# Kernel tuning notes

Measured on AMD Instinct MI355X. Metric: run time of the kernel, lower is better.

## Reference

```python
import jax, jax.numpy as jnp
import numpy as np
import math

B = 65536
N_NUM = 64; N_CAT = 16; CAT_SIZE = 1000; EMB = 16
ND = 64; NA = 64; OUT = ND + NA; NSTEPS = 5; GAMMA = 1.5
NFEAT = N_NUM + N_CAT * EMB          # 320
NGROUPS = N_NUM + N_CAT              # 80
GROUP_IDX = np.repeat(np.arange(NGROUPS), [1] * N_NUM + [EMB] * N_CAT)  # len 320
RES_SCALE = math.sqrt(0.5)
BN_EPS = 1e-5


def setup_inputs() -> dict:
    keys = iter(jax.random.split(jax.random.key(0), 64))
    def rn(shape, std):
        return jax.random.normal(next(keys), shape, jnp.float32) * std
    def mk_bn(c, lead=()):
        # stacked (scale, bias, running_mean, running_var) along axis -2
        s = 1.0 + 0.05 * jax.random.normal(next(keys), (*lead, c), jnp.float32)
        b = 0.05 * jax.random.normal(next(keys), (*lead, c), jnp.float32)
        m = 0.05 * jax.random.normal(next(keys), (*lead, c), jnp.float32)
        v = 1.0 + 0.1 * jax.random.uniform(next(keys), (*lead, c), dtype=jnp.float32)
        return jnp.stack([s, b, m, v], axis=-2)
    inp = {}
    inp["x_num"] = jax.random.normal(next(keys), (B, N_NUM), jnp.float32)
    inp["x_cat"] = jax.random.randint(next(keys), (B, N_CAT), 0, CAT_SIZE)
    inp["emb_W"] = rn((N_CAT, CAT_SIZE, EMB), 0.1)
    inp["in_bn"] = mk_bn(NFEAT)
    inp["sh_W0"] = rn((NFEAT, 2 * OUT), 1.0 / math.sqrt(NFEAT))
    inp["sh_b0"] = jnp.zeros((2 * OUT,), jnp.float32)
    inp["sh_bn0"] = mk_bn(2 * OUT)
    inp["sh_W1"] = rn((OUT, 2 * OUT), 1.0 / math.sqrt(OUT))
    inp["sh_b1"] = jnp.zeros((2 * OUT,), jnp.float32)
    inp["sh_bn1"] = mk_bn(2 * OUT)
    inp["init_W"] = rn((2, OUT, 2 * OUT), 1.0 / math.sqrt(OUT))
    inp["init_b"] = jnp.zeros((2, 2 * OUT), jnp.float32)
    inp["init_bn"] = mk_bn(2 * OUT, (2,))
    inp["step_W"] = rn((NSTEPS, 2, OUT, 2 * OUT), 1.0 / math.sqrt(OUT))
    inp["step_b"] = jnp.zeros((NSTEPS, 2, 2 * OUT), jnp.float32)
    inp["step_bn"] = mk_bn(2 * OUT, (NSTEPS, 2))
    inp["att_W"] = rn((NSTEPS, NA, NGROUPS), 1.0 / math.sqrt(NA))
    inp["att_b"] = jnp.zeros((NSTEPS, NGROUPS), jnp.float32)
    inp["att_bn"] = mk_bn(NGROUPS, (NSTEPS,))
    inp["out_W"] = rn((ND, 1), 1.0 / math.sqrt(ND))
    inp["out_b"] = jnp.zeros((1,), jnp.float32)
    return inp


def bn_apply(x, p):
    s, b, m, v = p  # each [C]
    return (x - m) * jax.lax.rsqrt(v + BN_EPS) * s + b


def glu_layer(x, W, b, bn):
    h = bn_apply(x @ W + b, bn)          # [B, 2*OUT]
    o, g = jnp.split(h, 2, axis=1)
    return o * jax.nn.sigmoid(g)


def glu_block(x, W, b, bn):
    y = glu_layer(x, W, b, bn)
    return (x + y) * RES_SCALE if x.shape == y.shape else y


def sparsemax(z):
    # along axis=1; Martins & Astudillo 2016
    zs = -jnp.sort(-z, axis=1)
    cs = jnp.cumsum(zs, axis=1)
    r = jnp.arange(1, z.shape[1] + 1, dtype=z.dtype)
    support = (1.0 + r * zs) > cs
    k = jnp.maximum(support.sum(axis=1, keepdims=True), 1)
    cs_k = jnp.take_along_axis(cs, k - 1, axis=1)
    tau = (cs_k - 1.0) / k.astype(z.dtype)
    return jnp.maximum(z - tau, 0.0)


def _forward(x_num, x_cat, emb_W, in_bn, sh_W0, sh_b0, sh_bn0, sh_W1, sh_b1, sh_bn1,
             init_W, init_b, init_bn, step_W, step_b, step_bn, att_W, att_b, att_bn,
             out_W, out_b):
    # categorical embeddings: [B, N_CAT, EMB] -> [B, N_CAT*EMB]
    emb = emb_W[np.arange(N_CAT)[None, :], x_cat].reshape(x_cat.shape[0], -1)
    x = jnp.concatenate([x_num, emb], axis=1)  # [B, NFEAT]
    x = bn_apply(x, in_bn)

    def ft_shared(h):
        h = glu_block(h, sh_W0, sh_b0, sh_bn0)   # 320 -> 128, no residual
        return glu_block(h, sh_W1, sh_b1, sh_bn1)  # residual

    def ft_indep(h, W, b, bn):
        for i in range(W.shape[0]):
            h = glu_block(h, W[i], b[i], bn[i])
        return h

    out0 = ft_indep(ft_shared(x), init_W, init_b, init_bn)
    a = out0[:, ND:]
    prior = jnp.ones((x.shape[0], NGROUPS), x.dtype)
    decision_sum = jnp.zeros((x.shape[0], ND), x.dtype)
    for step in range(NSTEPS):
        logits = bn_apply(a @ att_W[step] + att_b[step], att_bn[step]) * prior
        mask_group = sparsemax(logits)           # [B, NGROUPS]
        prior = prior * (GAMMA - mask_group)
        mask = mask_group[:, GROUP_IDX]          # [B, NFEAT] (repeat_interleave)
        out = ft_indep(ft_shared(mask * x), step_W[step], step_b[step], step_bn[step])
        d, a = out[:, :ND], out[:, ND:]
        decision_sum = decision_sum + jax.nn.relu(d)
    return decision_sum @ out_W + out_b          # [B, 1]


def reference(x_num, x_cat, emb_W, in_bn, sh_W0, sh_b0, sh_bn0, sh_W1, sh_b1, sh_bn1,
              init_W, init_b, init_bn, step_W, step_b, step_bn, att_W, att_b, att_bn,
              out_W, out_b):
    return _forward(x_num, x_cat, emb_W, in_bn, sh_W0, sh_b0, sh_bn0, sh_W1, sh_b1,
                    sh_bn1, init_W, init_b, init_bn, step_W, step_b, step_bn,
                    att_W, att_b, att_bn, out_W, out_b)
```

## Files before the change

### kernel.cpp

```cpp
#include <hip/hip_runtime.h>
#include <math.h>
#include <stdint.h>

typedef _Float16 half_t;
typedef _Float16 half8 __attribute__((ext_vector_type(8)));
typedef float floatx4 __attribute__((ext_vector_type(4)));
typedef float floatx16 __attribute__((ext_vector_type(16)));

constexpr float BN_EPS_C = 1e-5f;
constexpr float RES_SCALE_C = 0.70710678118654752f;
constexpr float GAMMA_C = 1.5f;
#define B_TOT 65536

__device__ __forceinline__ uint32_t pack2(float y) {
    const half_t h = (half_t)y;
    const half_t l = (half_t)(y - (float)h);
    union { half_t f; unsigned short u; } a, b; a.f = h; b.f = l;
    return (uint32_t)a.u | ((uint32_t)b.u << 16);
}
__device__ __forceinline__ void unpack2(uint32_t v, half_t& h, half_t& l) {
    union { unsigned short u; half_t f; } a, b;
    a.u = (unsigned short)(v & 0xffffu); b.u = (unsigned short)(v >> 16);
    h = a.f; l = b.f;
}

__global__ void wsplit_kernel(const float* __restrict__ sh_W0, const float* __restrict__ sh_W1,
                              const float* __restrict__ init_W, const float* __restrict__ step_W,
                              half_t* __restrict__ Wh, half_t* __restrict__ Wl)
{
    const int b = blockIdx.x, n = threadIdx.x;
    const float* src; int k; size_t base;
    if (b < 320)      { src = sh_W0;           k = b;       base = 0; }
    else if (b < 448) { src = sh_W1;           k = b - 320; base = 81920; }
    else if (b < 576) { src = init_W;          k = b - 448; base = 114688; }
    else if (b < 704) { src = init_W + 32768;  k = b - 576; base = 147456; }
    else {
        int j = (b - 704) >> 7; k = (b - 704) & 127;
        src = step_W + (size_t)j * 32768; base = 180224 + (size_t)j * 32768;
    }
    const float v = src[k * 256 + n];
    const half_t hi = (half_t)v;
    const half_t lo = (half_t)(v - (float)hi);
    const size_t idx = base + (size_t)(((k >> 3) * 256 + n) * 8 + (k & 7));
    Wh[idx] = hi; Wl[idx] = lo;
}

__global__ void wsplit_att_kernel(const float* __restrict__ att_W,
                                  half_t* __restrict__ aWh, half_t* __restrict__ aWl)
{
    const int b = blockIdx.x;
    const int n = threadIdx.x;
    const int step = b >> 6, k = b & 63;
    const float v = att_W[(size_t)b * 80 + n];
    const half_t h = (half_t)v;
    const half_t l = (half_t)(v - (float)h);
    const size_t idx = (size_t)step * 5120 + (size_t)(((k >> 3) * 80 + n) * 8 + (k & 7));
    aWh[idx] = h; aWl[idx] = l;
}

__global__ void embed_bn_kernel(const float* __restrict__ x_num, const int* __restrict__ x_cat,
                                const float* __restrict__ emb_W, const float* __restrict__ in_bn,
                                uint32_t* __restrict__ xp)
{
    const int idx = blockIdx.x * 256 + threadIdx.x;
    const int s = idx / 320, j = idx - s * 320;
    float v;
    if (j < 64) v = x_num[(size_t)s * 64 + j];
    else {
        const int c = (j - 64) >> 4, e = (j - 64) & 15;
        v = emb_W[(size_t)(c * 1000 + x_cat[(size_t)s * 16 + c]) * 16 + e];
    }
    const float val = (v - in_bn[640 + j]) * (in_bn[j] * __frsqrt_rn(in_bn[960 + j] + BN_EPS_C)) + in_bn[320 + j];
    xp[idx] = pack2(val);
}

__device__ __forceinline__ void bn_fold(const float* __restrict__ bn, const float* __restrict__ bias,
                                        int c, float& sc, float& sh)
{
    sc = bn[c] * __frsqrt_rn(bn[768 + c] + BN_EPS_C);
    sh = fmaf(bias[c] - bn[512 + c], sc, bn[256 + c]);
}

__device__ __forceinline__ float glu_val(float accO, float accG,
                                         float sc_o, float sh_o, float sc_g, float sh_g)
{
    const float o = fmaf(accO, sc_o, sh_o);
    const float g = fmaf(accG, sc_g, sh_g);
    const float e = __expf(-g);
    return o * __builtin_amdgcn_rcpf(1.f + e);
}

#define MFMA32(A, B, C) C = __builtin_amdgcn_mfma_f32_32x32x16_f16(A, B, C, 0, 0, 0)
#define MFMA16(A, B, C) C = __builtin_amdgcn_mfma_f32_16x16x32_f16(A, B, C, 0, 0, 0)

__device__ __forceinline__ void layer_accum(const half_t (*H_h)[136], const half_t (*H_l)[136],
                                            const half_t* __restrict__ Wh, const half_t* __restrict__ Wl,
                                            size_t off, int n32, int k8, int no, int rot,
                                            floatx16* accO, floatx16* accG)
{
#pragma unroll 1
    for (int s = 0; s < 8; ++s) {
        const int sl8 = (s + rot) & 7;
        const int kq = sl8 * 2 + k8;
        const size_t wo = off + (size_t)(kq * 256 + no + n32) * 8;
        const half8 bo_h = *(const half8*)(Wh + wo);
        const half8 bo_l = *(const half8*)(Wl + wo);
        const half8 bg_h = *(const half8*)(Wh + wo + 1024);
        const half8 bg_l = *(const half8*)(Wl + wo + 1024);
#pragma unroll
        for (int mt = 0; mt < 4; ++mt) {
            const half8 a_h = *(const half8*)&H_h[mt * 32 + n32][sl8 * 16 + k8 * 8];
            const half8 a_l = *(const half8*)&H_l[mt * 32 + n32][sl8 * 16 + k8 * 8];
            MFMA32(a_h, bo_h, accO[mt]); MFMA32(a_h, bg_h, accG[mt]);
            MFMA32(a_l, bo_h, accO[mt]); MFMA32(a_l, bg_h, accG[mt]);
            MFMA32(a_h, bo_l, accO[mt]); MFMA32(a_h, bg_l, accG[mt]);
        }
    }
}

template<bool MASK>
__global__ __launch_bounds__(256, 2)
void ft_chain(const uint32_t* __restrict__ xp, uint32_t* __restrict__ avp,
              const half_t* __restrict__ Wh, const half_t* __restrict__ Wl,
              const half_t* __restrict__ aWh, const half_t* __restrict__ aWl,
              const float* __restrict__ att_b, const float* __restrict__ att_bn,
              float* __restrict__ prior,
              const float* __restrict__ b1, const float* __restrict__ bn1,
              const float* __restrict__ b2, const float* __restrict__ bn2,
              const float* __restrict__ b3, const float* __restrict__ bn3,
              const float* __restrict__ b4, const float* __restrict__ bn4,
              size_t w3_off, size_t w4_off,
              float* __restrict__ ds, int wmode_last, int step)
{
    __shared__ __align__(16) char smem[79872];
    float    (*mgs)[84]  = (float    (*)[84])smem;
    half_t   (*As_h)[72] = (half_t   (*)[72])(smem + 43008);
    half_t   (*As_l)[72] = (half_t   (*)[72])(smem + 61440);
    uint32_t (*Apk)[68]  = (uint32_t (*)[68])(smem + 43008);
    half_t   (*H_h)[136] = (half_t   (*)[136])smem;
    half_t   (*H_l)[136] = (half_t   (*)[136])(smem + 34816);

    const int t = threadIdx.x;
    const int s0 = blockIdx.x * 128;
    const int w = t >> 6, lane = t & 63;
    const int n32 = lane & 31, k8 = lane >> 5;
    const int quad = lane >> 4, l16 = lane & 15;
    const int no = 32 * w;
    const int half_id = (blockIdx.x >> 8) & 1;
    const int row = t >> 1, k0 = (t & 1) * 32;

    if (MASK) {
        {
            const uint4* src = (const uint4*)(avp + (size_t)(s0 + row) * 64 + k0);
            uint4* dst = (uint4*)&Apk[row][k0];
#pragma unroll
            for (int q = 0; q < 8; ++q) dst[q] = src[q];
        }
        __syncthreads();
        floatx4 zacc[2][5];
#pragma unroll
        for (int mt = 0; mt < 2; ++mt)
#pragma unroll
            for (int nt = 0; nt < 5; ++nt) zacc[mt][nt] = (floatx4){0.f, 0.f, 0.f, 0.f};
#pragma unroll
        for (int kc = 0; kc < 64; kc += 32) {
            half8 a_h[2], a_l[2];
#pragma unroll
            for (int mt = 0; mt < 2; ++mt) {
                uint32_t wv[8];
                *(uint4*)&wv[0] = *(const uint4*)&Apk[w * 32 + mt * 16 + l16][kc + quad * 8];
                *(uint4*)&wv[4] = *(const uint4*)&Apk[w * 32 + mt * 16 + l16][kc + quad * 8 + 4];
#pragma unroll
                for (int j = 0; j < 8; ++j) { half_t h, l; unpack2(wv[j], h, l); a_h[mt][j] = h; a_l[mt][j] = l; }
            }
            const int kq = (kc >> 3) + quad;
#pragma unroll
            for (int nt = 0; nt < 5; ++nt) {
                const size_t wi = (size_t)(kq * 80 + nt * 16 + l16) * 8;
                const half8 b_h = *(const half8*)(aWh + wi);
                const half8 b_l = *(const half8*)(aWl + wi);
#pragma unroll
                for (int mt = 0; mt < 2; ++mt) {
                    MFMA16(a_h[mt], b_h, zacc[mt][nt]);
                    MFMA16(a_l[mt], b_h, zacc[mt][nt]);
                    MFMA16(a_h[mt], b_l, zacc[mt][nt]);
                }
            }
        }
        float preg[2][5][4];
#pragma unroll
        for (int nt = 0; nt < 5; ++nt) {
            const int c = nt * 16 + l16;
            const float sc = att_bn[c] * __frsqrt_rn(att_bn[240 + c] + BN_EPS_C);
            const float sh = fmaf(att_b[c] - att_bn[160 + c], sc, att_bn[80 + c]);
#pragma unroll
            for (int mt = 0; mt < 2; ++mt)
#pragma unroll
                for (int r = 0; r < 4; ++r) {
                    const int sl = w * 32 + mt * 16 + quad * 4 + r;
                    const float pr = (step == 0) ? 1.f : prior[(size_t)(s0 + sl) * 80 + c];
                    preg[mt][nt][r] = pr;
                    mgs[sl][c] = fmaf(zacc[mt][nt][r], sc, sh) * pr;
                }
        }
        __syncthreads();
        {
            const int samp = row, j0 = (t & 1) * 40;
            float zj[40], zmax = -1e30f;
#pragma unroll
            for (int j = 0; j < 40; ++j) { zj[j] = mgs[samp][j0 + j]; zmax = fmaxf(zmax, zj[j]); }
            zmax = fmaxf(zmax, __shfl_xor(zmax, 1));
            float lo = zmax - 1.f, hi = zmax;
#pragma unroll 1
            for (int it = 0; it < 22; ++it) {
                const float mid = 0.5f * (lo + hi);
                float ssum = 0.f;
#pragma unroll
                for (int j = 0; j < 40; ++j) ssum += fmaxf(zj[j] - mid, 0.f);
                ssum += __shfl_xor(ssum, 1);
                if (ssum >= 1.f) lo = mid; else hi = mid;
            }
            const float tau = 0.5f * (lo + hi);
#pragma unroll
            for (int j = 0; j < 40; ++j) mgs[samp][j0 + j] = fmaxf(zj[j] - tau, 0.f);
        }
        __syncthreads();
#pragma unroll
        for (int nt = 0; nt < 5; ++nt) {
            const int c = nt * 16 + l16;
#pragma unroll
            for (int mt = 0; mt < 2; ++mt)
#pragma unroll
                for (int r = 0; r < 4; ++r) {
                    const int sl = w * 32 + mt * 16 + quad * 4 + r;
                    prior[(size_t)(s0 + sl) * 80 + c] = preg[mt][nt][r] * (GAMMA_C - mgs[sl][c]);
                }
        }
    }

    floatx16 accO[4], accG[4];
#pragma unroll
    for (int i = 0; i < 4; ++i) { accO[i] = (floatx16)(0.f); accG[i] = (floatx16)(0.f); }

    const uint32_t* arow = xp + (size_t)(s0 + row) * 320 + k0;
    uint32_t pfw[32];
    int ic = half_id * 2;
#pragma unroll
    for (int q = 0; q < 8; ++q)
        *(uint4*)&pfw[q * 4] = *(const uint4*)(arow + ic * 64 + q * 4);

#pragma unroll 1
    for (int i = 0; i < 5; ++i) {
        __syncthreads();
        {
            const int kb = ic * 64 + k0;
            float mA = 1.f, mB = 1.f;
            if (MASK && ic != 0) {
                mA = mgs[row][64 + ((kb - 64) >> 4)];
                mB = mgs[row][64 + ((kb - 48) >> 4)];
            }
#pragma unroll
            for (int q = 0; q < 4; ++q) {
                half8 hh, ll;
                if (MASK && ic == 0) {
                    const float4 m0q = *(const float4*)&mgs[row][kb + q * 8];
                    const float4 m1q = *(const float4*)&mgs[row][kb + q * 8 + 4];
                    const float mm[8] = {m0q.x, m0q.y, m0q.z, m0q.w, m1q.x, m1q.y, m1q.z, m1q.w};
#pragma unroll
                    for (int j = 0; j < 8; ++j) {
                        half_t h, l; unpack2(pfw[q * 8 + j], h, l);
                        const float v = ((float)h + (float)l) * mm[j];
                        const half_t nh = (half_t)v;
                        hh[j] = nh; ll[j] = (half_t)(v - (float)nh);
                    }
                } else if (MASK) {
                    const float m = (q < 2) ? mA : mB;
#pragma unroll
                    for (int j = 0; j < 8; ++j) {
                        half_t h, l; unpack2(pfw[q * 8 + j], h, l);
                        const float v = ((float)h + (float)l) * m;
                        const half_t nh = (half_t)v;
                        hh[j] = nh; ll[j] = (half_t)(v - (float)nh);
                    }
                } else {
#pragma unroll
                    for (int j = 0; j < 8; ++j) { half_t h, l; unpack2(pfw[q * 8 + j], h, l); hh[j] = h; ll[j] = l; }
                }
                *(half8*)&As_h[row][k0 + q * 8] = hh;
                *(half8*)&As_l[row][k0 + q * 8] = ll;
            }
        }
        __syncthreads();
        const int icn = (ic + 1 == 5) ? 0 : ic + 1;
        if (i < 4) {
#pragma unroll
            for (int q = 0; q < 8; ++q)
                *(uint4*)&pfw[q * 4] = *(const uint4*)(arow + icn * 64 + q * 4);
        }
#pragma unroll
        for (int sl4 = 0; sl4 < 4; ++sl4) {
            const int kq = ic * 8 + sl4 * 2 + k8;
            const size_t wo = (size_t)(kq * 256 + no + n32) * 8;
            const half8 bo_h = *(const half8*)(Wh + wo);
            const half8 bo_l = *(const half8*)(Wl + wo);
            const half8 bg_h = *(const half8*)(Wh + wo + 1024);
            const half8 bg_l = *(const half8*)(Wl + wo + 1024);
#pragma unroll
            for (int mt = 0; mt < 4; ++mt) {
                const half8 a_h = *(const half8*)&As_h[mt * 32 + n32][sl4 * 16 + k8 * 8];
                const half8 a_l = *(const half8*)&As_l[mt * 32 + n32][sl4 * 16 + k8 * 8];
                MFMA32(a_h, bo_h, accO[mt]); MFMA32(a_h, bg_h, accG[mt]);
                MFMA32(a_l, bo_h, accO[mt]); MFMA32(a_l, bg_h, accG[mt]);
                MFMA32(a_h, bo_l, accO[mt]); MFMA32(a_h, bg_l, accG[mt]);
            }
        }
        ic = icn;
    }
    __syncthreads();

    {
        const int c = no + n32;
        float sc_o, sh_o, sc_g, sh_g;
        bn_fold(bn1, b1, c, sc_o, sh_o);
        bn_fold(bn1, b1, c + 128, sc_g, sh_g);
#pragma unroll
        for (int mt = 0; mt < 4; ++mt)
#pragma unroll
            for (int reg = 0; reg < 16; ++reg) {
                const int sl = mt * 32 + (reg & 3) + 8 * (reg >> 2) + 4 * k8;
                const float y = glu_val(accO[mt][reg], accG[mt][reg], sc_o, sh_o, sc_g, sh_g);
                const half_t nh = (half_t)y;
                H_h[sl][c] = nh; H_l[sl][c] = (half_t)(y - (float)nh);
            }
    }
    __syncthreads();

#pragma unroll 1
    for (int layer = 0; layer < 2; ++layer) {
        const float* bb = layer ? b3 : b2;
        const float* bn = layer ? bn3 : bn2;
        const size_t off = layer ? w3_off : (size_t)81920;
#pragma unroll
        for (int i = 0; i < 4; ++i) { accO[i] = (floatx16)(0.f); accG[i] = (floatx16)(0.f); }
        layer_accum(H_h, H_l, Wh, Wl, off, n32, k8, no, half_id * 4, accO, accG);
        __syncthreads();
        {
            const int c = no + n32;
            float sc_o, sh_o, sc_g, sh_g;
            bn_fold(bn, bb, c, sc_o, sh_o);
            bn_fold(bn, bb, c + 128, sc_g, sh_g);
#pragma unroll
            for (int mt = 0; mt < 4; ++mt)
#pragma unroll
                for (int reg = 0; reg < 16; ++reg) {
                    const int sl = mt * 32 + (reg & 3) + 8 * (reg >> 2) + 4 * k8;
                    const float res = (float)H_h[sl][c] + (float)H_l[sl][c];
                    const float y = (glu_val(accO[mt][reg], accG[mt][reg], sc_o, sh_o, sc_g, sh_g) + res) * RES_SCALE_C;
                    const half_t nh = (half_t)y;
                    H_h[sl][c] = nh; H_l[sl][c] = (half_t)(y - (float)nh);
                }
        }
        __syncthreads();
    }

#pragma unroll
    for (int i = 0; i < 4; ++i) { accO[i] = (floatx16)(0.f); accG[i] = (floatx16)(0.f); }
    layer_accum(H_h, H_l, Wh, Wl, w4_off, n32, k8, no, half_id * 4, accO, accG);
    {
        const int c = no + n32;
        float sc_o, sh_o, sc_g, sh_g;
        bn_fold(bn4, b4, c, sc_o, sh_o);
        bn_fold(bn4, b4, c + 128, sc_g, sh_g);
        if (w < 2) {
            if (wmode_last != 1) {
#pragma unroll
                for (int mt = 0; mt < 4; ++mt)
#pragma unroll
                    for (int reg = 0; reg < 16; ++reg) {
                        const int sl = mt * 32 + (reg & 3) + 8 * (reg >> 2) + 4 * k8;
                        const float res = (float)H_h[sl][c] + (float)H_l[sl][c];
                        const float y = (glu_val(accO[mt][reg], accG[mt][reg], sc_o, sh_o, sc_g, sh_g) + res) * RES_SCALE_C;
                        const float d = fmaxf(y, 0.f);
                        float* dp = ds + (size_t)(s0 + sl) * 64 + c;
                        *dp = (wmode_last == 2) ? d : (*dp + d);
                    }
            }
        } else {
#pragma unroll
            for (int mt = 0; mt < 4; ++mt)
#pragma unroll
                for (int reg = 0; reg < 16; ++reg) {
                    const int sl = mt * 32 + (reg & 3) + 8 * (reg >> 2) + 4 * k8;
                    const float res = (float)H_h[sl][c] + (float)H_l[sl][c];
                    const float y = (glu_val(accO[mt][reg], accG[mt][reg], sc_o, sh_o, sc_g, sh_g) + res) * RES_SCALE_C;
                    avp[(size_t)(s0 + sl) * 64 + (c - 64)] = pack2(y);
                }
        }
    }
}

__global__ void final_kernel(const float* __restrict__ dsum, const float* __restrict__ out_W,
                             const float* __restrict__ out_b, float* __restrict__ out)
{
    const int s = blockIdx.x * 256 + threadIdx.x;
    float acc = out_b[0];
    const float4* dp = (const float4*)(dsum + (size_t)s * 64);
    const float4* wp = (const float4*)out_W;
#pragma unroll
    for (int q = 0; q < 16; ++q) {
        const float4 d = dp[q];
        const float4 ww = wp[q];
        acc += d.x * ww.x + d.y * ww.y + d.z * ww.z + d.w * ww.w;
    }
    out[s] = acc;
}

extern "C" void kernel_launch(void* const* d_in, const int* in_sizes, int n_in,
                              void* d_out, int out_size, void* d_ws, size_t ws_size,
                              hipStream_t stream)
{
    const float* x_num  = (const float*)d_in[0];
    const int*   x_cat  = (const int*)d_in[1];
    const float* emb_W  = (const float*)d_in[2];
    const float* in_bn  = (const float*)d_in[3];
    const float* sh_W0  = (const float*)d_in[4];
    const float* sh_b0  = (const float*)d_in[5];
    const float* sh_bn0 = (const float*)d_in[6];
    const float* sh_W1  = (const float*)d_in[7];
    const float* sh_b1  = (const float*)d_in[8];
    const float* sh_bn1 = (const float*)d_in[9];
    const float* init_W = (const float*)d_in[10];
    const float* init_b = (const float*)d_in[11];
    const float* init_bn= (const float*)d_in[12];
    const float* step_W = (const float*)d_in[13];
    const float* step_b = (const float*)d_in[14];
    const float* step_bn= (const float*)d_in[15];
    const float* att_W  = (const float*)d_in[16];
    const float* att_b  = (const float*)d_in[17];
    const float* att_bn = (const float*)d_in[18];
    const float* out_W  = (const float*)d_in[19];
    const float* out_b  = (const float*)d_in[20];

    const size_t B = B_TOT;
    char* p = (char*)d_ws;
    uint32_t* xp  = (uint32_t*)p;  p += B * 320 * 4;
    uint32_t* avp = (uint32_t*)p;  p += B * 64 * 4;
    half_t* Wh    = (half_t*)p;    p += 507904 * 2;
    half_t* Wl    = (half_t*)p;    p += 507904 * 2;
    half_t* aWh   = (half_t*)p;    p += 25600 * 2;
    half_t* aWl   = (half_t*)p;    p += 25600 * 2;
    float* pri    = (float*)p;     p += B * 80 * 4;
    float* ds     = (float*)p;     p += B * 64 * 4;

    wsplit_kernel<<<1984, 256, 0, stream>>>(sh_W0, sh_W1, init_W, step_W, Wh, Wl);
    wsplit_att_kernel<<<320, 80, 0, stream>>>(att_W, aWh, aWl);
    embed_bn_kernel<<<(B_TOT * 320) / 256, 256, 0, stream>>>(x_num, x_cat, emb_W, in_bn, xp);

    const int GB = B_TOT / 128;
    ft_chain<false><<<GB, 256, 0, stream>>>(xp, avp, Wh, Wl,
                                            nullptr, nullptr, nullptr, nullptr, nullptr,
                                            sh_b0, sh_bn0, sh_b1, sh_bn1,
                                            init_b, init_bn, init_b + 256, init_bn + 1024,
                                            (size_t)114688, (size_t)147456, ds, 1, 0);
    for (int st = 0; st < 5; ++st) {
        const size_t w3 = 180224 + (size_t)(st * 2 + 0) * 32768;
        const size_t w4 = 180224 + (size_t)(st * 2 + 1) * 32768;
        ft_chain<true><<<GB, 256, 0, stream>>>(xp, avp, Wh, Wl,
                                               aWh + st * 5120, aWl + st * 5120,
                                               att_b + st * 80, att_bn + st * 320, pri,
                                               sh_b0, sh_bn0, sh_b1, sh_bn1,
                                               step_b + (st * 2 + 0) * 256, step_bn + (st * 2 + 0) * 1024,
                                               step_b + (st * 2 + 1) * 256, step_bn + (st * 2 + 1) * 1024,
                                               w3, w4, ds, st == 0 ? 2 : 3, st);
    }
    final_kernel<<<B_TOT / 256, 256, 0, stream>>>(ds, out_W, out_b, (float*)d_out);
}
```

Measured before the change: 778.5 us.

## Double-buffer MFMA operand loads and use lighter barriers with packed fp16 splits

Result: slower. 859.2 us (+10.4%).

```diff
diff --git a/kernel.cpp b/kernel.cpp
--- a/kernel.cpp
+++ b/kernel.cpp
@@ -4,6 +4,7 @@
 
 typedef _Float16 half_t;
 typedef _Float16 half8 __attribute__((ext_vector_type(8)));
+typedef __fp16 fp16x2 __attribute__((ext_vector_type(2)));
 typedef float floatx4 __attribute__((ext_vector_type(4)));
 typedef float floatx16 __attribute__((ext_vector_type(16)));
 
@@ -11,6 +12,10 @@
 constexpr float RES_SCALE_C = 0.70710678118654752f;
 constexpr float GAMMA_C = 1.5f;
 #define B_TOT 65536
+
+__device__ __forceinline__ void lgkm_barrier() {
+    __asm__ volatile("s_waitcnt lgkmcnt(0)\n\ts_barrier" ::: "memory");
+}
 
 __device__ __forceinline__ uint32_t pack2(float y) {
     const half_t h = (half_t)y;
@@ -22,6 +27,19 @@
     union { unsigned short u; half_t f; } a, b;
     a.u = (unsigned short)(v & 0xffffu); b.u = (unsigned short)(v >> 16);
     h = a.f; l = b.f;
+}
+__device__ __forceinline__ void split_pair(float y0, float y1, half_t& h0, half_t& l0, half_t& h1, half_t& l1) {
+    fp16x2 hh = __builtin_amdgcn_cvt_pkrtz(y0, y1);
+    fp16x2 ll = __builtin_amdgcn_cvt_pkrtz(y0 - (float)hh.x, y1 - (float)hh.y);
+    h0 = (half_t)hh.x; l0 = (half_t)ll.x; h1 = (half_t)hh.y; l1 = (half_t)ll.y;
+}
+__device__ __forceinline__ void pack2_pair(float y0, float y1, uint32_t& w0, uint32_t& w1) {
+    fp16x2 hh = __builtin_amdgcn_cvt_pkrtz(y0, y1);
+    fp16x2 ll = __builtin_amdgcn_cvt_pkrtz(y0 - (float)hh.x, y1 - (float)hh.y);
+    const uint32_t hb = __builtin_bit_cast(uint32_t, hh);
+    const uint32_t lb = __builtin_bit_cast(uint32_t, ll);
+    w0 = (hb & 0xffffu) | (lb << 16);
+    w1 = (hb >> 16) | (lb & 0xffff0000u);
 }
 
 __global__ void wsplit_kernel(const float* __restrict__ sh_W0, const float* __restrict__ sh_W1,
@@ -98,22 +116,42 @@
                                             size_t off, int n32, int k8, int no, int rot,
                                             floatx16* accO, floatx16* accG)
 {
-#pragma unroll 1
+    half8 bo_h[2], bg_h[2], bo_l[2], bg_l[2];
+    half8 a_h[2][4], a_l[2][4];
+    {
+        const int sl8 = rot & 7;
+        const size_t wo = off + (size_t)((sl8 * 2 + k8) * 256 + no + n32) * 8;
+        bo_h[0] = *(const half8*)(Wh + wo);
+        bg_h[0] = *(const half8*)(Wh + wo + 1024);
+        bo_l[0] = *(const half8*)(Wl + wo);
+        bg_l[0] = *(const half8*)(Wl + wo + 1024);
+#pragma unroll
+        for (int mt = 0; mt < 4; ++mt) {
+            a_h[0][mt] = *(const half8*)&H_h[mt * 32 + n32][sl8 * 16 + k8 * 8];
+            a_l[0][mt] = *(const half8*)&H_l[mt * 32 + n32][sl8 * 16 + k8 * 8];
+        }
+    }
+#pragma unroll
     for (int s = 0; s < 8; ++s) {
-        const int sl8 = (s + rot) & 7;
-        const int kq = sl8 * 2 + k8;
-        const size_t wo = off + (size_t)(kq * 256 + no + n32) * 8;
-        const half8 bo_h = *(const half8*)(Wh + wo);
-        const half8 bo_l = *(const half8*)(Wl + wo);
-        const half8 bg_h = *(const half8*)(Wh + wo + 1024);
-        const half8 bg_l = *(const half8*)(Wl + wo + 1024);
+        const int cur = s & 1, nxt = cur ^ 1;
+        if (s < 7) {
+            const int nsl = (s + 1 + rot) & 7;
+            const size_t wo = off + (size_t)((nsl * 2 + k8) * 256 + no + n32) * 8;
+            bo_h[nxt] = *(const half8*)(Wh + wo);
+            bg_h[nxt] = *(const half8*)(Wh + wo + 1024);
+            bo_l[nxt] = *(const half8*)(Wl + wo);
+            bg_l[nxt] = *(const half8*)(Wl + wo + 1024);
+#pragma unroll
+            for (int mt = 0; mt < 4; ++mt) {
+                a_h[nxt][mt] = *(const half8*)&H_h[mt * 32 + n32][nsl * 16 + k8 * 8];
+                a_l[nxt][mt] = *(const half8*)&H_l[mt * 32 + n32][nsl * 16 + k8 * 8];
+            }
+        }
 #pragma unroll
         for (int mt = 0; mt < 4; ++mt) {
-            const half8 a_h = *(const half8*)&H_h[mt * 32 + n32][sl8 * 16 + k8 * 8];
-            const half8 a_l = *(const half8*)&H_l[mt * 32 + n32][sl8 * 16 + k8 * 8];
-            MFMA32(a_h, bo_h, accO[mt]); MFMA32(a_h, bg_h, accG[mt]);
-            MFMA32(a_l, bo_h, accO[mt]); MFMA32(a_l, bg_h, accG[mt]);
-            MFMA32(a_h, bo_l, accO[mt]); MFMA32(a_h, bg_l, accG[mt]);
+            MFMA32(a_h[cur][mt], bo_h[cur], accO[mt]); MFMA32(a_h[cur][mt], bg_h[cur], accG[mt]);
+            MFMA32(a_l[cur][mt], bo_h[cur], accO[mt]); MFMA32(a_l[cur][mt], bg_h[cur], accG[mt]);
+            MFMA32(a_h[cur][mt], bo_l[cur], accO[mt]); MFMA32(a_h[cur][mt], bg_l[cur], accG[mt]);
         }
     }
 }
@@ -156,7 +194,7 @@
 #pragma unroll
             for (int q = 0; q < 8; ++q) dst[q] = src[q];
         }
-        __syncthreads();
+        lgkm_barrier();
         floatx4 zacc[2][5];
 #pragma unroll
         for (int mt = 0; mt < 2; ++mt)
@@ -203,7 +241,7 @@
                     mgs[sl][c] = fmaf(zacc[mt][nt][r], sc, sh) * pr;
                 }
         }
-        __syncthreads();
+        lgkm_barrier();
         {
             const int samp = row, j0 = (t & 1) * 40;
             float zj[40], zmax = -1e30f;
@@ -224,7 +262,7 @@
 #pragma unroll
             for (int j = 0; j < 40; ++j) mgs[samp][j0 + j] = fmaxf(zj[j] - tau, 0.f);
         }
-        __syncthreads();
+        lgkm_barrier();
 #pragma unroll
         for (int nt = 0; nt < 5; ++nt) {
             const int c = nt * 16 + l16;
@@ -249,9 +287,19 @@
     for (int q = 0; q < 8; ++q)
         *(uint4*)&pfw[q * 4] = *(const uint4*)(arow + ic * 64 + q * 4);
 
+    half8 wbo_h[2], wbg_h[2], wbo_l[2], wbg_l[2];
+
 #pragma unroll 1
     for (int i = 0; i < 5; ++i) {
-        __syncthreads();
+        {
+            const int kq = ic * 8 + k8;
+            const size_t wo = (size_t)(kq * 256 + no + n32) * 8;
+            wbo_h[0] = *(const half8*)(Wh + wo);
+            wbg_h[0] = *(const half8*)(Wh + wo + 1024);
+            wbo_l[0] = *(const half8*)(Wl + wo);
+            wbg_l[0] = *(const half8*)(Wl + wo + 1024);
+        }
+        lgkm_barrier();
         {
             const int kb = ic * 64 + k0;
             float mA = 1.f, mB = 1.f;
@@ -290,7 +338,7 @@
                 *(half8*)&As_l[row][k0 + q * 8] = ll;
             }
         }
-        __syncthreads();
+        lgkm_barrier();
         const int icn = (ic + 1 == 5) ? 0 : ic + 1;
         if (i < 4) {
 #pragma unroll
@@ -299,24 +347,27 @@
         }
 #pragma unroll
         for (int sl4 = 0; sl4 < 4; ++sl4) {
-            const int kq = ic * 8 + sl4 * 2 + k8;
-            const size_t wo = (size_t)(kq * 256 + no + n32) * 8;
-            const half8 bo_h = *(const half8*)(Wh + wo);
-            const half8 bo_l = *(const half8*)(Wl + wo);
-            const half8 bg_h = *(const half8*)(Wh + wo + 1024);
-            const half8 bg_l = *(const half8*)(Wl + wo + 1024);
+            const int cur = sl4 & 1, nxt = cur ^ 1;
+            if (sl4 < 3) {
+                const int kq = ic * 8 + (sl4 + 1) * 2 + k8;
+                const size_t wo = (size_t)(kq * 256 + no + n32) * 8;
+                wbo_h[nxt] = *(const half8*)(Wh + wo);
+                wbg_h[nxt] = *(const half8*)(Wh + wo + 1024);
+                wbo_l[nxt] = *(const half8*)(Wl + wo);
+                wbg_l[nxt] = *(const half8*)(Wl + wo + 1024);
+            }
 #pragma unroll
             for (int mt = 0; mt < 4; ++mt) {
                 const half8 a_h = *(const half8*)&As_h[mt * 32 + n32][sl4 * 16 + k8 * 8];
                 const half8 a_l = *(const half8*)&As_l[mt * 32 + n32][sl4 * 16 + k8 * 8];
-                MFMA32(a_h, bo_h, accO[mt]); MFMA32(a_h, bg_h, accG[mt]);
-                MFMA32(a_l, bo_h, accO[mt]); MFMA32(a_l, bg_h, accG[mt]);
-                MFMA32(a_h, bo_l, accO[mt]); MFMA32(a_h, bg_l, accG[mt]);
+                MFMA32(a_h, wbo_h[cur], accO[mt]); MFMA32(a_h, wbg_h[cur], accG[mt]);
+                MFMA32(a_l, wbo_h[cur], accO[mt]); MFMA32(a_l, wbg_h[cur], accG[mt]);
+                MFMA32(a_h, wbo_l[cur], accO[mt]); MFMA32(a_h, wbg_l[cur], accG[mt]);
             }
         }
         ic = icn;
     }
-    __syncthreads();
+    lgkm_barrier();
 
     {
         const int c = no + n32;
@@ -326,14 +377,20 @@
 #pragma unroll
         for (int mt = 0; mt < 4; ++mt)
 #pragma unroll
-            for (int reg = 0; reg < 16; ++reg) {
-                const int sl = mt * 32 + (reg & 3) + 8 * (reg >> 2) + 4 * k8;
-                const float y = glu_val(accO[mt][reg], accG[mt][reg], sc_o, sh_o, sc_g, sh_g);
-                const half_t nh = (half_t)y;
-                H_h[sl][c] = nh; H_l[sl][c] = (half_t)(y - (float)nh);
-            }
-    }
-    __syncthreads();
+            for (int q = 0; q < 4; ++q)
+#pragma unroll
+                for (int rp = 0; rp < 2; ++rp) {
+                    const int r0 = q * 4 + rp * 2;
+                    const int sl = mt * 32 + rp * 2 + 8 * q + 4 * k8;
+                    const float y0 = glu_val(accO[mt][r0],     accG[mt][r0],     sc_o, sh_o, sc_g, sh_g);
+                    const float y1 = glu_val(accO[mt][r0 + 1], accG[mt][r0 + 1], sc_o, sh_o, sc_g, sh_g);
+                    half_t h0, l0, h1, l1;
+                    split_pair(y0, y1, h0, l0, h1, l1);
+                    H_h[sl][c] = h0; H_l[sl][c] = l0;
+                    H_h[sl + 1][c] = h1; H_l[sl + 1][c] = l1;
+                }
+    }
+    lgkm_barrier();
 
 #pragma unroll 1
     for (int layer = 0; layer < 2; ++layer) {
@@ -343,7 +400,7 @@
 #pragma unroll
         for (int i = 0; i < 4; ++i) { accO[i] = (floatx16)(0.f); accG[i] = (floatx16)(0.f); }
         layer_accum(H_h, H_l, Wh, Wl, off, n32, k8, no, half_id * 4, accO, accG);
-        __syncthreads();
+        lgkm_barrier();
         {
             const int c = no + n32;
             float sc_o, sh_o, sc_g, sh_g;
@@ -352,15 +409,22 @@
 #pragma unroll
             for (int mt = 0; mt < 4; ++mt)
 #pragma unroll
-                for (int reg = 0; reg < 16; ++reg) {
-                    const int sl = mt * 32 + (reg & 3) + 8 * (reg >> 2) + 4 * k8;
-                    const float res = (float)H_h[sl][c] + (float)H_l[sl][c];
-                    const float y = (glu_val(accO[mt][reg], accG[mt][reg], sc_o, sh_o, sc_g, sh_g) + res) * RES_SCALE_C;
-                    const half_t nh = (half_t)y;
-                    H_h[sl][c] = nh; H_l[sl][c] = (half_t)(y - (float)nh);
-                }
-        }
-        __syncthreads();
+                for (int q = 0; q < 4; ++q)
+#pragma unroll
+                    for (int rp = 0; rp < 2; ++rp) {
+                        const int r0 = q * 4 + rp * 2;
+                        const int sl = mt * 32 + rp * 2 + 8 * q + 4 * k8;
+                        const float res0 = (float)H_h[sl][c] + (float)H_l[sl][c];
+                        const float res1 = (float)H_h[sl + 1][c] + (float)H_l[sl + 1][c];
+                        const float y0 = (glu_val(accO[mt][r0],     accG[mt][r0],     sc_o, sh_o, sc_g, sh_g) + res0) * RES_SCALE_C;
+                        const float y1 = (glu_val(accO[mt][r0 + 1], accG[mt][r0 + 1], sc_o, sh_o, sc_g, sh_g) + res1) * RES_SCALE_C;
+                        half_t h0, l0, h1, l1;
+                        split_pair(y0, y1, h0, l0, h1, l1);
+                        H_h[sl][c] = h0; H_l[sl][c] = l0;
+                        H_h[sl + 1][c] = h1; H_l[sl + 1][c] = l1;
+                    }
+        }
+        lgkm_barrier();
     }
 
 #pragma unroll
@@ -389,12 +453,20 @@
 #pragma unroll
             for (int mt = 0; mt < 4; ++mt)
 #pragma unroll
-                for (int reg = 0; reg < 16; ++reg) {
-                    const int sl = mt * 32 + (reg & 3) + 8 * (reg >> 2) + 4 * k8;
-                    const float res = (float)H_h[sl][c] + (float)H_l[sl][c];
-                    const float y = (glu_val(accO[mt][reg], accG[mt][reg], sc_o, sh_o, sc_g, sh_g) + res) * RES_SCALE_C;
-                    avp[(size_t)(s0 + sl) * 64 + (c - 64)] = pack2(y);
-                }
+                for (int q = 0; q < 4; ++q)
+#pragma unroll
+                    for (int rp = 0; rp < 2; ++rp) {
+                        const int r0 = q * 4 + rp * 2;
+                        const int sl = mt * 32 + rp * 2 + 8 * q + 4 * k8;
+                        const float res0 = (float)H_h[sl][c] + (float)H_l[sl][c];
+                        const float res1 = (float)H_h[sl + 1][c] + (float)H_l[sl + 1][c];
+                        const float y0 = (glu_val(accO[mt][r0],     accG[mt][r0],     sc_o, sh_o, sc_g, sh_g) + res0) * RES_SCALE_C;
+                        const float y1 = (glu_val(accO[mt][r0 + 1], accG[mt][r0 + 1], sc_o, sh_o, sc_g, sh_g) + res1) * RES_SCALE_C;
+                        uint32_t w0, w1;
+                        pack2_pair(y0, y1, w0, w1);
+                        avp[(size_t)(s0 + sl) * 64 + (c - 64)] = w0;
+                        avp[(size_t)(s0 + sl + 1) * 64 + (c - 64)] = w1;
+                    }
         }
     }
 }
```
